# Performance work log

Measured on AMD Instinct MI355X. Metric: run time of the kernel, lower is better.

Reference implementation:

```python
import jax, jax.numpy as jnp
import numpy as np


def setup_inputs() -> dict:
    key = jax.random.key(0)
    ks = jax.random.split(key, 5)
    B, T, E, C = 4, 1024, 4, 512
    IN, OUT = 2048, 8192
    return {
        "x": jax.random.normal(ks[0], (B, T, IN), dtype=jnp.float32),
        "combine_array": jax.random.uniform(ks[1], (B, T, E, C), dtype=jnp.float32),
        "dispatch_mask": jax.random.uniform(ks[2], (B, T, E, C), dtype=jnp.float32),
        "weight": jax.random.normal(ks[3], (OUT, IN), dtype=jnp.float32) * 0.02,
        "bias": jax.random.normal(ks[4], (OUT,), dtype=jnp.float32) * 0.02,
        "num_experts": E,
    }


def reference(x, combine_array, dispatch_mask, weight, bias, num_experts):
    E = num_experts
    i = weight.shape[1] // E  # expert_in_features
    w = weight.reshape(E, -1, i)  # (E, out, i) -- same reshape as torch
    B = x.shape[0]
    xr = x.reshape(B, -1, E, i)  # (B, T, E, i)
    # dispatch: gather tokens into expert capacity slots via dense mask
    xd = jnp.einsum('btei,btec->beci', xr, dispatch_mask)  # (B, E, C, i)
    # homogeneous coordinates to fold bias into the matmul (as in original)
    x_homo = jnp.concatenate([xd, jnp.ones_like(xd[..., :1])], axis=-1)  # (B,E,C,i+1)
    b_col = jnp.broadcast_to(bias.reshape(1, -1, 1), (E, w.shape[1], 1))
    w_homo = jnp.concatenate([w, b_col], axis=-1)  # (E, out, i+1)
    # per-expert matmul then combine back to tokens
    y = jnp.einsum('beci,eoi->beco', x_homo, w_homo)  # (B, E, C, out)
    return jnp.einsum('beco,btec->bto', y, combine_array)  # (B, T, out)
```

## Files before the change

### kernel.cpp

```cpp
#include <hip/hip_runtime.h>

#define B_   4
#define T_   1024
#define E_   4
#define C_   512
#define IN_  2048
#define OUT_ 8192
#define EI_  512

typedef float f32x4 __attribute__((ext_vector_type(4)));
typedef __bf16 bf16x8 __attribute__((ext_vector_type(8)));
typedef unsigned short ushort8 __attribute__((ext_vector_type(8)));

__device__ __forceinline__ unsigned short f32_bf16(float f) {
  unsigned int u = __float_as_uint(f);
  u += 0x7FFFu + ((u >> 16) & 1u);
  return (unsigned short)(u >> 16);
}

__device__ __forceinline__ void gl2lds16(const void* g, void* l) {
  __builtin_amdgcn_global_load_lds(
      (const __attribute__((address_space(1))) void*)g,
      (__attribute__((address_space(3))) void*)l, 16, 0, 0);
}

__global__ __launch_bounds__(256)
void transpose_cvt(const float* __restrict__ src, unsigned short* __restrict__ dst) {
  __shared__ float tile[64][68];
  const int b = blockIdx.z;
  const int k0 = blockIdx.x * 64;
  const int t0 = blockIdx.y * 64;
  const int u = threadIdx.x;
  const int lrow = u >> 4;
  const int lcol = (u & 15) * 4;
  const float* s = src + (size_t)b * (T_ * 2048) + (size_t)t0 * 2048 + k0;
#pragma unroll
  for (int r = 0; r < 4; r++) {
    float4 v = *(const float4*)(s + (size_t)(lrow + 16 * r) * 2048 + lcol);
    tile[lrow + 16 * r][lcol]     = v.x;
    tile[lrow + 16 * r][lcol + 1] = v.y;
    tile[lrow + 16 * r][lcol + 2] = v.z;
    tile[lrow + 16 * r][lcol + 3] = v.w;
  }
  __syncthreads();
  const int w = u >> 6, lane = u & 63;
  const int kg = k0 + lane;
  const int e  = kg >> 9;
  const int kl = kg & 511;
  unsigned short* d = dst + (((size_t)b * 4 + e) * 512 + kl) * 1024 + t0 + w * 16;
#pragma unroll
  for (int s8 = 0; s8 < 2; s8++) {
    const int tt = w * 16 + s8 * 8;
    ushort8 r;
#pragma unroll
    for (int j = 0; j < 8; j++) r[j] = f32_bf16(tile[tt + j][lane]);
    *(ushort8*)(d + s8 * 8) = r;
  }
}

__global__ __launch_bounds__(256)
void cvt_combine_rowsum(const float* __restrict__ in,
                        unsigned short* __restrict__ out,
                        float* __restrict__ S) {
  const int row = blockIdx.x;
  const int u = threadIdx.x;
  const float4* p = (const float4*)(in + (size_t)row * 2048) + (size_t)u * 2;
  float4 a = p[0], b = p[1];
  ushort8 r;
  r[0] = f32_bf16(a.x); r[1] = f32_bf16(a.y);
  r[2] = f32_bf16(a.z); r[3] = f32_bf16(a.w);
  r[4] = f32_bf16(b.x); r[5] = f32_bf16(b.y);
  r[6] = f32_bf16(b.z); r[7] = f32_bf16(b.w);
  *((ushort8*)(out + (size_t)row * 2048) + u) = r;
  float s = (a.x + a.y + a.z + a.w) + (b.x + b.y + b.z + b.w);
  __shared__ float red[256];
  red[u] = s;
  __syncthreads();
#pragma unroll
  for (int st = 128; st > 0; st >>= 1) {
    if (u < st) red[u] += red[u + st];
    __syncthreads();
  }
  if (u == 0) S[row] = red[0];
}

__global__ __launch_bounds__(256)
void permute_w(const float* __restrict__ weight, unsigned short* __restrict__ W2) {
  const int tid = blockIdx.x * 256 + threadIdx.x;
  const int i8 = tid & 63;
  const int e  = (tid >> 6) & 3;
  const int o  = tid >> 8;
  const float* s = weight + (size_t)e * 4194304 + (size_t)o * 512 + i8 * 8;
  float4 a = *(const float4*)s;
  float4 b = *(const float4*)(s + 4);
  ushort8 r;
  r[0] = f32_bf16(a.x); r[1] = f32_bf16(a.y);
  r[2] = f32_bf16(a.z); r[3] = f32_bf16(a.w);
  r[4] = f32_bf16(b.x); r[5] = f32_bf16(b.y);
  r[6] = f32_bf16(b.z); r[7] = f32_bf16(b.w);
  *(ushort8*)(W2 + (size_t)o * 2048 + e * 512 + i8 * 8) = r;
}

template <int MODE>
__global__ __launch_bounds__(256, 2)
void gemm_bt(const unsigned short* __restrict__ A,
             const unsigned short* __restrict__ Bm,
             void* __restrict__ Out, const float* __restrict__ bias,
             const float* __restrict__ S,
             int lda, int ldb, int ldo, int K, int Ediv,
             long sAb, long sAe, long sBb, long sBe, long sOb, long sOe) {
  __shared__ __align__(16) unsigned short As[128 * 32];
  __shared__ __align__(16) unsigned short Bs[128 * 32];
  const int u = threadIdx.x;
  const int z = blockIdx.z;
  const int zb = z / Ediv, ze = z % Ediv;
  const unsigned short* Ab = A  + zb * sAb + ze * sAe + (long)(blockIdx.y * 128) * lda;
  const unsigned short* Bb = Bm + zb * sBb + ze * sBe + (long)(blockIdx.x * 128) * ldb;

  const int srow = u >> 2;
  const int scol = (u & 3) * 8;
  const unsigned short* ga0 = Ab + (long)srow * lda + scol;
  const unsigned short* ga1 = ga0 + (long)64 * lda;
  const unsigned short* gb0 = Bb + (long)srow * ldb + scol;
  const unsigned short* gb1 = gb0 + (long)64 * ldb;

  const int w = u >> 6, lane = u & 63;
  unsigned short* la0 = As + w * 512;
  unsigned short* la1 = la0 + 2048;
  unsigned short* lb0 = Bs + w * 512;
  unsigned short* lb1 = lb0 + 2048;

  const int wm = (w & 1) * 64, wn = (w >> 1) * 64;
  const int fm = lane & 15, fk = (lane >> 4) * 8;
  const unsigned short* pA = As + (wm + fm) * 32 + fk;
  const unsigned short* pB = Bs + (wn + fm) * 32 + fk;

  f32x4 acc[4][4] = {};

  for (int kt = 0; kt < K; kt += 32) {
    __syncthreads();
    gl2lds16(ga0, la0);
    gl2lds16(ga1, la1);
    gl2lds16(gb0, lb0);
    gl2lds16(gb1, lb1);
    ga0 += 32; ga1 += 32; gb0 += 32; gb1 += 32;
    __syncthreads();
    bf16x8 af[4], bfv[4];
#pragma unroll
    for (int i = 0; i < 4; i++) {
      af[i]  = *(const bf16x8*)(pA + i * 16 * 32);
      bfv[i] = *(const bf16x8*)(pB + i * 16 * 32);
    }
#pragma unroll
    for (int i = 0; i < 4; i++)
#pragma unroll
      for (int j = 0; j < 4; j++)
        acc[i][j] = __builtin_amdgcn_mfma_f32_16x16x32_bf16(af[i], bfv[j],
                                                            acc[i][j], 0, 0, 0);
  }

  const long ob = zb * sOb + ze * sOe;
  const int em0 = blockIdx.y * 128 + wm + ((lane >> 4) << 2);
  const int en0 = blockIdx.x * 128 + wn + (lane & 15);
  float bcol[4];
  if (MODE == 1) {
#pragma unroll
    for (int j = 0; j < 4; j++) bcol[j] = bias[en0 + j * 16];
  }
#pragma unroll
  for (int i = 0; i < 4; i++)
#pragma unroll
    for (int r = 0; r < 4; r++) {
      const int m = em0 + i * 16 + r;
      const float sm = (MODE == 1) ? S[m] : 0.0f;
#pragma unroll
      for (int j = 0; j < 4; j++) {
        const long off = ob + (long)m * ldo + en0 + j * 16;
        if (MODE == 1)
          ((float*)Out)[off] = acc[i][j][r] + sm * bcol[j];
        else
          ((unsigned short*)Out)[off] = f32_bf16(acc[i][j][r]);
      }
    }
}

#define DSR(dst, addr) do { f32x4 _t_; \
    asm volatile("ds_read_b128 %0, %1" : "=v"(_t_) : "v"(addr)); \
    dst = __builtin_bit_cast(bf16x8, _t_); } while (0)

__global__ __launch_bounds__(512, 2)
void gemm256(const unsigned short* __restrict__ A,
             const unsigned short* __restrict__ Bm,
             float* __restrict__ Out,
             const float* __restrict__ bias,
             const float* __restrict__ S) {
  __shared__ __align__(16) unsigned short lds[65536];
  char* ldsg = (char*)lds;
  const unsigned ldsb =
      (unsigned)(unsigned long long)(__attribute__((address_space(3))) char*)(void*)lds;

  int wg = blockIdx.x;
  wg = (wg & 7) * 64 + (wg >> 3);
  const int bx = wg & 31;
  const int by = wg >> 5;

  const int u = threadIdx.x;
  const int w = u >> 6, lane = u & 63;
  const unsigned w1024 = (unsigned)(w * 1024);
  const int wmw = (w >> 2) * 128;
  const int wnw = (w & 3) * 64;
  const int fm = lane & 15;

  const unsigned hi16  = (unsigned)(((lane >> 4) & 3) * 16);
  const unsigned xorv  = (unsigned)((fm & 7) << 4);
  const unsigned colS0 = hi16 ^ xorv;
  const unsigned aR0 = (unsigned)((wmw + fm) * 128) + colS0;
  const unsigned aR1 = aR0 ^ 64u;
  const unsigned bR0 = 65536u + (unsigned)((wnw + fm) * 128) + colS0;
  const unsigned bR1 = bR0 ^ 64u;

  const int srr = w * 8 + (lane >> 3);
  const unsigned swzS = (unsigned)((((lane & 7) ^ ((lane >> 3) & 7)) << 4));
  const char* gA = (const char*)(A  + (size_t)(by * 256) * 2048) + (size_t)srr * 4096 + swzS;
  const char* gB = (const char*)(Bm + (size_t)(bx * 256) * 2048) + (size_t)srr * 4096 + swzS;

#define STG(gsrc, loff) do { \
    gl2lds16((gsrc), ldsg + (loff)); \
    gl2lds16((gsrc) + 262144, ldsg + (loff) + 8192); } while (0)

  STG(gA,                    0u + w1024);
  STG(gA + 524288,       16384u + w1024);
  STG(gB,                65536u + w1024);
  STG(gB + 524288,       81920u + w1024);
  STG(gA + 128,          32768u + w1024);
  STG(gA + 128 + 524288, 49152u + w1024);
  asm volatile("s_waitcnt vmcnt(4)" ::: "memory");
  __builtin_amdgcn_s_barrier();

  f32x4 acc[8][4] = {};
  bf16x8 a0[4][2], a1[4][2], bq[2][2];

  for (int kt = 0; kt < 32; ++kt) {
    const unsigned bbO = (unsigned)((kt & 1) * 32768);
    const unsigned nbR = bbO ^ 32768u;
    const int ktB = (kt + 1 < 32) ? kt + 1 : 31;
    const int ktA = (kt + 2 < 32) ? kt + 2 : 31;
    const char* gBn = gB + ktB * 128;
    const char* gAn = gA + ktA * 128;

#pragma unroll
    for (int i = 0; i < 4; ++i) {
      DSR(a0[i][0], ldsb + bbO + aR0 + (unsigned)(i * 2048));
      DSR(a0[i][1], ldsb + bbO + aR1 + (unsigned)(i * 2048));
    }
#pragma unroll
    for (int j = 0; j < 2; ++j) {
      DSR(bq[j][0], ldsb + bbO + bR0 + (unsigned)(j * 2048));
      DSR(bq[j][1], ldsb + bbO + bR1 + (unsigned)(j * 2048));
    }
    STG(gBn, 65536u + nbR + w1024);
    __builtin_amdgcn_s_barrier();
    asm volatile("s_waitcnt lgkmcnt(0)" ::: "memory");
    __builtin_amdgcn_sched_barrier(0);
    __builtin_amdgcn_s_setprio(1);
#pragma unroll
    for (int i = 0; i < 4; ++i)
#pragma unroll
      for (int j = 0; j < 2; ++j) {
        acc[i][j] = __builtin_amdgcn_mfma_f32_16x16x32_bf16(a0[i][0], bq[j][0], acc[i][j], 0, 0, 0);
        acc[i][j] = __builtin_amdgcn_mfma_f32_16x16x32_bf16(a0[i][1], bq[j][1], acc[i][j], 0, 0, 0);
      }
    __builtin_amdgcn_s_setprio(0);
    __builtin_amdgcn_s_barrier();

#pragma unroll
    for (int i = 0; i < 4; ++i) {
      DSR(a1[i][0], ldsb + bbO + aR0 + (unsigned)((4 + i) * 2048));
      DSR(a1[i][1], ldsb + bbO + aR1 + (unsigned)((4 + i) * 2048));
    }
    STG(gBn + 524288, 81920u + nbR + w1024);
    __builtin_amdgcn_s_barrier();
    asm volatile("s_waitcnt lgkmcnt(0)" ::: "memory");
    __builtin_amdgcn_sched_barrier(0);
    __builtin_amdgcn_s_setprio(1);
#pragma unroll
    for (int i = 0; i < 4; ++i)
#pragma unroll
      for (int j = 0; j < 2; ++j) {
        acc[4 + i][j] = __builtin_amdgcn_mfma_f32_16x16x32_bf16(a1[i][0], bq[j][0], acc[4 + i][j], 0, 0, 0);
        acc[4 + i][j] = __builtin_amdgcn_mfma_f32_16x16x32_bf16(a1[i][1], bq[j][1], acc[4 + i][j], 0, 0, 0);
      }
    __builtin_amdgcn_s_setprio(0);
    __builtin_amdgcn_s_barrier();

#pragma unroll
    for (int j = 0; j < 2; ++j) {
      DSR(bq[j][0], ldsb + bbO + bR0 + (unsigned)((2 + j) * 2048));
      DSR(bq[j][1], ldsb + bbO + bR1 + (unsigned)((2 + j) * 2048));
    }
    STG(gAn, bbO + w1024);
    __builtin_amdgcn_s_barrier();
    asm volatile("s_waitcnt lgkmcnt(0)" ::: "memory");
    __builtin_amdgcn_sched_barrier(0);
    __builtin_amdgcn_s_setprio(1);
#pragma unroll
    for (int i = 0; i < 4; ++i)
#pragma unroll
      for (int j = 0; j < 2; ++j) {
        acc[i][2 + j] = __builtin_amdgcn_mfma_f32_16x16x32_bf16(a0[i][0], bq[j][0], acc[i][2 + j], 0, 0, 0);
        acc[i][2 + j] = __builtin_amdgcn_mfma_f32_16x16x32_bf16(a0[i][1], bq[j][1], acc[i][2 + j], 0, 0, 0);
      }
    __builtin_amdgcn_s_setprio(0);
    __builtin_amdgcn_s_barrier();

    STG(gAn + 524288, bbO + 16384u + w1024);
    __builtin_amdgcn_s_barrier();
    __builtin_amdgcn_s_setprio(1);
#pragma unroll
    for (int i = 0; i < 4; ++i)
#pragma unroll
      for (int j = 0; j < 2; ++j) {
        acc[4 + i][2 + j] = __builtin_amdgcn_mfma_f32_16x16x32_bf16(a1[i][0], bq[j][0], acc[4 + i][2 + j], 0, 0, 0);
        acc[4 + i][2 + j] = __builtin_amdgcn_mfma_f32_16x16x32_bf16(a1[i][1], bq[j][1], acc[4 + i][2 + j], 0, 0, 0);
      }
    __builtin_amdgcn_s_setprio(0);
    asm volatile("s_waitcnt vmcnt(4)" ::: "memory");
    __builtin_amdgcn_sched_barrier(0);
    __builtin_amdgcn_s_barrier();
  }
#undef STG

  const int m0 = by * 256 + wmw + ((lane >> 4) << 2);
  const int n0 = bx * 256 + wnw + (lane & 15);
  float bc[4];
#pragma unroll
  for (int j = 0; j < 4; ++j) bc[j] = bias[n0 + j * 16];
#pragma unroll
  for (int i = 0; i < 8; ++i)
#pragma unroll
    for (int r = 0; r < 4; ++r) {
      const int m = m0 + i * 16 + r;
      const float sm = S[m];
#pragma unroll
      for (int j = 0; j < 4; ++j)
        Out[(size_t)m * 8192 + n0 + j * 16] = acc[i][j][r] + sm * bc[j];
    }
}

extern "C" void kernel_launch(void* const* d_in, const int* in_sizes, int n_in,
                              void* d_out, int out_size, void* d_ws,
                              size_t ws_size, hipStream_t stream) {
  (void)in_sizes; (void)n_in; (void)out_size; (void)ws_size;
  const float* x       = (const float*)d_in[0];
  const float* combine = (const float*)d_in[1];
  const float* mask    = (const float*)d_in[2];
  const float* weight  = (const float*)d_in[3];
  const float* bias    = (const float*)d_in[4];
  float* out = (float*)d_out;

  char* ws = (char*)d_ws;
  unsigned short* W2      = (unsigned short*)ws;
  unsigned short* comb_bf = (unsigned short*)(ws + 33554432);
  float*          S       = (float*)(ws + 50331648);
  unsigned short* xT      = (unsigned short*)(ws + 51380224);
  unsigned short* maskT   = (unsigned short*)(ws + 68157440);
  unsigned short* xdT     = (unsigned short*)(ws + 84934656);
  unsigned short* zbuf    = (unsigned short*)(ws + 93323264);

  transpose_cvt<<<dim3(32, 16, 4), 256, 0, stream>>>(x, xT);
  transpose_cvt<<<dim3(32, 16, 4), 256, 0, stream>>>(mask, maskT);
  cvt_combine_rowsum<<<4096, 256, 0, stream>>>(combine, comb_bf, S);
  permute_w<<<8192, 256, 0, stream>>>(weight, W2);

  gemm_bt<0><<<dim3(4, 4, 16), 256, 0, stream>>>(
      xT, maskT, (void*)xdT, nullptr, nullptr, 1024, 1024, 512, 1024,
      4, 2097152L, 524288L, 2097152L, 524288L, 1048576L, 262144L);

  gemm_bt<0><<<dim3(4, 8, 16), 256, 0, stream>>>(
      comb_bf, xdT, (void*)zbuf, nullptr, nullptr, 2048, 512, 2048, 512,
      4, 2097152L, 512L, 1048576L, 262144L, 2097152L, 512L);

  gemm256<<<dim3(512), 512, 0, stream>>>(zbuf, W2, out, bias, S);
}
```

Baseline: 425.6 us.

## Fuse preprocessing kernels, double-buffer gemm_bt LDS, and retune transpose store pattern

Merges the four preprocessing kernels (two transposes, combine conversion with row sums, weight permute) into a single launch that dispatches on block index, removing launch gaps. The transpose now uses a 65-wide padded tile and a different thread-to-output mapping. gemm_bt gets double-buffered LDS so the next K tile's global-to-LDS loads overlap the current MFMAs, dropping one barrier per iteration. A vmcnt(0) wait is also added before the gemm256 epilogue. Risks include more LDS per block in gemm_bt and the prefetch relying on implicit waits before the barrier.

```diff
diff --git a/kernel.cpp b/kernel.cpp
--- a/kernel.cpp
+++ b/kernel.cpp
@@ -25,80 +25,83 @@
 }
 
 __global__ __launch_bounds__(256)
-void transpose_cvt(const float* __restrict__ src, unsigned short* __restrict__ dst) {
-  __shared__ float tile[64][68];
-  const int b = blockIdx.z;
-  const int k0 = blockIdx.x * 64;
-  const int t0 = blockIdx.y * 64;
+void prep(const float* __restrict__ xsrc, const float* __restrict__ msrc,
+          const float* __restrict__ combine, const float* __restrict__ weight,
+          unsigned short* __restrict__ xdst, unsigned short* __restrict__ mdst,
+          unsigned short* __restrict__ comb_bf, float* __restrict__ S,
+          unsigned short* __restrict__ W2) {
+  const int bid = blockIdx.x;
   const int u = threadIdx.x;
-  const int lrow = u >> 4;
-  const int lcol = (u & 15) * 4;
-  const float* s = src + (size_t)b * (T_ * 2048) + (size_t)t0 * 2048 + k0;
-#pragma unroll
-  for (int r = 0; r < 4; r++) {
-    float4 v = *(const float4*)(s + (size_t)(lrow + 16 * r) * 2048 + lcol);
-    tile[lrow + 16 * r][lcol]     = v.x;
-    tile[lrow + 16 * r][lcol + 1] = v.y;
-    tile[lrow + 16 * r][lcol + 2] = v.z;
-    tile[lrow + 16 * r][lcol + 3] = v.w;
+  if (bid < 4096) {
+    __shared__ float tile[64][65];
+    const int z = bid >> 9;
+    const int which = z >> 2;
+    const int b = z & 3;
+    const int rem = bid & 511;
+    const int t0 = (rem >> 5) * 64;
+    const int k0 = (rem & 31) * 64;
+    const float* src = which ? msrc : xsrc;
+    unsigned short* dst = which ? mdst : xdst;
+    const int lrow = u >> 4;
+    const int lcol = (u & 15) * 4;
+    const float* s = src + (size_t)b * (T_ * 2048) + (size_t)t0 * 2048 + k0;
+#pragma unroll
+    for (int r = 0; r < 4; r++) {
+      float4 v = *(const float4*)(s + (size_t)(lrow + 16 * r) * 2048 + lcol);
+      tile[lrow + 16 * r][lcol]     = v.x;
+      tile[lrow + 16 * r][lcol + 1] = v.y;
+      tile[lrow + 16 * r][lcol + 2] = v.z;
+      tile[lrow + 16 * r][lcol + 3] = v.w;
+    }
+    __syncthreads();
+    const int kr = u >> 2;
+    const int tq = (u & 3) * 8;
+    const int kg = k0 + kr;
+    const int e  = kg >> 9;
+    const int kl = kg & 511;
+    unsigned short* d = dst + (((size_t)b * 4 + e) * 512 + kl) * 1024 + t0 + tq;
+#pragma unroll
+    for (int s8 = 0; s8 < 2; s8++) {
+      ushort8 rr;
+#pragma unroll
+      for (int j = 0; j < 8; j++) rr[j] = f32_bf16(tile[tq + s8 * 32 + j][kr]);
+      *(ushort8*)(d + s8 * 32) = rr;
+    }
+  } else if (bid < 8192) {
+    __shared__ float red[256];
+    const int row = bid - 4096;
+    const float4* p = (const float4*)(combine + (size_t)row * 2048) + (size_t)u * 2;
+    float4 a = p[0], b = p[1];
+    ushort8 r;
+    r[0] = f32_bf16(a.x); r[1] = f32_bf16(a.y);
+    r[2] = f32_bf16(a.z); r[3] = f32_bf16(a.w);
+    r[4] = f32_bf16(b.x); r[5] = f32_bf16(b.y);
+    r[6] = f32_bf16(b.z); r[7] = f32_bf16(b.w);
+    *((ushort8*)(comb_bf + (size_t)row * 2048) + u) = r;
+    float s = (a.x + a.y + a.z + a.w) + (b.x + b.y + b.z + b.w);
+    red[u] = s;
+    __syncthreads();
+#pragma unroll
+    for (int st = 128; st > 0; st >>= 1) {
+      if (u < st) red[u] += red[u + st];
+      __syncthreads();
+    }
+    if (u == 0) S[row] = red[0];
+  } else {
+    const int tid = (bid - 8192) * 256 + u;
+    const int i8 = tid & 63;
+    const int e  = (tid >> 6) & 3;
+    const int o  = tid >> 8;
+    const float* s = weight + (size_t)e * 4194304 + (size_t)o * 512 + i8 * 8;
+    float4 a = *(const float4*)s;
+    float4 b = *(const float4*)(s + 4);
+    ushort8 r;
+    r[0] = f32_bf16(a.x); r[1] = f32_bf16(a.y);
+    r[2] = f32_bf16(a.z); r[3] = f32_bf16(a.w);
+    r[4] = f32_bf16(b.x); r[5] = f32_bf16(b.y);
+    r[6] = f32_bf16(b.z); r[7] = f32_bf16(b.w);
+    *(ushort8*)(W2 + (size_t)o * 2048 + e * 512 + i8 * 8) = r;
   }
-  __syncthreads();
-  const int w = u >> 6, lane = u & 63;
-  const int kg = k0 + lane;
-  const int e  = kg >> 9;
-  const int kl = kg & 511;
-  unsigned short* d = dst + (((size_t)b * 4 + e) * 512 + kl) * 1024 + t0 + w * 16;
-#pragma unroll
-  for (int s8 = 0; s8 < 2; s8++) {
-    const int tt = w * 16 + s8 * 8;
-    ushort8 r;
-#pragma unroll
-    for (int j = 0; j < 8; j++) r[j] = f32_bf16(tile[tt + j][lane]);
-    *(ushort8*)(d + s8 * 8) = r;
-  }
-}
-
-__global__ __launch_bounds__(256)
-void cvt_combine_rowsum(const float* __restrict__ in,
-                        unsigned short* __restrict__ out,
-                        float* __restrict__ S) {
-  const int row = blockIdx.x;
-  const int u = threadIdx.x;
-  const float4* p = (const float4*)(in + (size_t)row * 2048) + (size_t)u * 2;
-  float4 a = p[0], b = p[1];
-  ushort8 r;
-  r[0] = f32_bf16(a.x); r[1] = f32_bf16(a.y);
-  r[2] = f32_bf16(a.z); r[3] = f32_bf16(a.w);
-  r[4] = f32_bf16(b.x); r[5] = f32_bf16(b.y);
-  r[6] = f32_bf16(b.z); r[7] = f32_bf16(b.w);
-  *((ushort8*)(out + (size_t)row * 2048) + u) = r;
-  float s = (a.x + a.y + a.z + a.w) + (b.x + b.y + b.z + b.w);
-  __shared__ float red[256];
-  red[u] = s;
-  __syncthreads();
-#pragma unroll
-  for (int st = 128; st > 0; st >>= 1) {
-    if (u < st) red[u] += red[u + st];
-    __syncthreads();
-  }
-  if (u == 0) S[row] = red[0];
-}
-
-__global__ __launch_bounds__(256)
-void permute_w(const float* __restrict__ weight, unsigned short* __restrict__ W2) {
-  const int tid = blockIdx.x * 256 + threadIdx.x;
-  const int i8 = tid & 63;
-  const int e  = (tid >> 6) & 3;
-  const int o  = tid >> 8;
-  const float* s = weight + (size_t)e * 4194304 + (size_t)o * 512 + i8 * 8;
-  float4 a = *(const float4*)s;
-  float4 b = *(const float4*)(s + 4);
-  ushort8 r;
-  r[0] = f32_bf16(a.x); r[1] = f32_bf16(a.y);
-  r[2] = f32_bf16(a.z); r[3] = f32_bf16(a.w);
-  r[4] = f32_bf16(b.x); r[5] = f32_bf16(b.y);
-  r[6] = f32_bf16(b.z); r[7] = f32_bf16(b.w);
-  *(ushort8*)(W2 + (size_t)o * 2048 + e * 512 + i8 * 8) = r;
 }
 
 template <int MODE>
@@ -109,8 +112,8 @@
              const float* __restrict__ S,
              int lda, int ldb, int ldo, int K, int Ediv,
              long sAb, long sAe, long sBb, long sBe, long sOb, long sOe) {
-  __shared__ __align__(16) unsigned short As[128 * 32];
-  __shared__ __align__(16) unsigned short Bs[128 * 32];
+  __shared__ __align__(16) unsigned short As[2][4096];
+  __shared__ __align__(16) unsigned short Bs[2][4096];
   const int u = threadIdx.x;
   const int z = blockIdx.z;
   const int zb = z / Ediv, ze = z % Ediv;
@@ -125,26 +128,33 @@
   const unsigned short* gb1 = gb0 + (long)64 * ldb;
 
   const int w = u >> 6, lane = u & 63;
-  unsigned short* la0 = As + w * 512;
-  unsigned short* la1 = la0 + 2048;
-  unsigned short* lb0 = Bs + w * 512;
-  unsigned short* lb1 = lb0 + 2048;
+  const int wq = w * 512;
 
   const int wm = (w & 1) * 64, wn = (w >> 1) * 64;
   const int fm = lane & 15, fk = (lane >> 4) * 8;
-  const unsigned short* pA = As + (wm + fm) * 32 + fk;
-  const unsigned short* pB = Bs + (wn + fm) * 32 + fk;
 
   f32x4 acc[4][4] = {};
 
-  for (int kt = 0; kt < K; kt += 32) {
-    __syncthreads();
-    gl2lds16(ga0, la0);
-    gl2lds16(ga1, la1);
-    gl2lds16(gb0, lb0);
-    gl2lds16(gb1, lb1);
-    ga0 += 32; ga1 += 32; gb0 += 32; gb1 += 32;
-    __syncthreads();
+  gl2lds16(ga0, As[0] + wq);
+  gl2lds16(ga1, As[0] + wq + 2048);
+  gl2lds16(gb0, Bs[0] + wq);
+  gl2lds16(gb1, Bs[0] + wq + 2048);
+  ga0 += 32; ga1 += 32; gb0 += 32; gb1 += 32;
+  __syncthreads();
+
+  const int nt = K / 32;
+  for (int t = 0; t < nt; ++t) {
+    const int cur = t & 1;
+    if (t + 1 < nt) {
+      const int nx = cur ^ 1;
+      gl2lds16(ga0, As[nx] + wq);
+      gl2lds16(ga1, As[nx] + wq + 2048);
+      gl2lds16(gb0, Bs[nx] + wq);
+      gl2lds16(gb1, Bs[nx] + wq + 2048);
+      ga0 += 32; ga1 += 32; gb0 += 32; gb1 += 32;
+    }
+    const unsigned short* pA = As[cur] + (wm + fm) * 32 + fk;
+    const unsigned short* pB = Bs[cur] + (wn + fm) * 32 + fk;
     bf16x8 af[4], bfv[4];
 #pragma unroll
     for (int i = 0; i < 4; i++) {
@@ -157,6 +167,7 @@
       for (int j = 0; j < 4; j++)
         acc[i][j] = __builtin_amdgcn_mfma_f32_16x16x32_bf16(af[i], bfv[j],
                                                             acc[i][j], 0, 0, 0);
+    __syncthreads();
   }
 
   const long ob = zb * sOb + ze * sOe;
@@ -329,6 +340,7 @@
     __builtin_amdgcn_s_barrier();
   }
 #undef STG
+  asm volatile("s_waitcnt vmcnt(0)" ::: "memory");
 
   const int m0 = by * 256 + wmw + ((lane >> 4) << 2);
   const int n0 = bx * 256 + wnw + (lane & 15);
@@ -367,10 +379,8 @@
   unsigned short* xdT     = (unsigned short*)(ws + 84934656);
   unsigned short* zbuf    = (unsigned short*)(ws + 93323264);
 
-  transpose_cvt<<<dim3(32, 16, 4), 256, 0, stream>>>(x, xT);
-  transpose_cvt<<<dim3(32, 16, 4), 256, 0, stream>>>(mask, maskT);
-  cvt_combine_rowsum<<<4096, 256, 0, stream>>>(combine, comb_bf, S);
-  permute_w<<<8192, 256, 0, stream>>>(weight, W2);
+  prep<<<16384, 256, 0, stream>>>(x, mask, combine, weight, xT, maskT,
+                                  comb_bf, S, W2);
 
   gemm_bt<0><<<dim3(4, 4, 16), 256, 0, stream>>>(
       xT, maskT, (void*)xdT, nullptr, nullptr, 1024, 1024, 512, 1024,
```

Measured after the change: 415.3 us. 1.02x faster.
